# Optimization experiments

Hardware: AMD Instinct MI355X
Metric: run time of the kernel (lower is better)

## Reference

```python
import jax, jax.numpy as jnp
import numpy as np

NEG_SLOPE = 0.2


def gat_conv(h_in, src, dst, W, attn_l, attn_r, num_nodes):
    """DGL-style GATConv: fc -> per-head attention logits -> edge softmax over dst -> scatter-add."""
    H, D = attn_l.shape
    h = (h_in @ W).reshape(num_nodes, H, D)                      # [N,H,D]
    el = jnp.sum(h * attn_l, axis=-1)                            # [N,H]
    er = jnp.sum(h * attn_r, axis=-1)                            # [N,H]
    e = jax.nn.leaky_relu(el[src] + er[dst], NEG_SLOPE)          # [E,H]
    m = jax.ops.segment_max(e, dst, num_segments=num_nodes)      # [N,H]
    m = jnp.where(jnp.isfinite(m), m, 0.0)                       # guard empty segments
    ex = jnp.exp(e - m[dst])                                     # [E,H]
    denom = jax.ops.segment_sum(ex, dst, num_segments=num_nodes) # [N,H]
    a = ex / denom[dst]                                          # [E,H]
    msg = h[src] * a[:, :, None]                                 # [E,H,D]
    out = jax.ops.segment_sum(msg, dst, num_segments=num_nodes)  # [N,H,D]
    return out.reshape(num_nodes, H * D)                         # concat heads


def setup_inputs() -> dict:
    key = jax.random.key(0)
    ks = jax.random.split(key, 12)
    N, E, G = 65536, 1048576, 512
    F_in, H, D = 128, 8, 32
    F_mid = H * D  # 256, concat agg mode
    P = 512
    inp = {
        "node_feats": jax.random.normal(ks[0], (N, F_in), jnp.float32),
        "src": jax.random.randint(ks[1], (E,), 0, N, jnp.int32),
        "dst": jax.random.randint(ks[2], (E,), 0, N, jnp.int32),
        "graph_ids": jnp.sort(jax.random.randint(ks[3], (N,), 0, G, jnp.int32)),
        "num_graphs": G,
        "W0": jax.random.normal(ks[4], (F_in, H * D), jnp.float32) * (1.0 / np.sqrt(F_in)),
        "al0": jax.random.normal(ks[5], (H, D), jnp.float32) * 0.1,
        "ar0": jax.random.normal(ks[6], (H, D), jnp.float32) * 0.1,
        "W1": jax.random.normal(ks[7], (F_mid, H * D), jnp.float32) * (1.0 / np.sqrt(F_mid)),
        "al1": jax.random.normal(ks[8], (H, D), jnp.float32) * 0.1,
        "ar1": jax.random.normal(ks[9], (H, D), jnp.float32) * 0.1,
        "Wd1": jax.random.normal(ks[10], (F_mid, P), jnp.float32) * (1.0 / np.sqrt(F_mid)),
        "bd1": jnp.zeros((P,), jnp.float32),
        "Wd2": jax.random.normal(ks[11], (P, 1), jnp.float32) * (1.0 / np.sqrt(P)),
        "bd2": jnp.zeros((1,), jnp.float32),
    }
    return inp


def reference(node_feats, src, dst, graph_ids, num_graphs,
              W0, al0, ar0, W1, al1, ar1, Wd1, bd1, Wd2, bd2):
    N = node_feats.shape[0]
    # two GATConv message-passing steps with concat head aggregation
    h = gat_conv(node_feats, src, dst, W0, al0, ar0, N)   # [N, 256]
    h = gat_conv(h, src, dst, W1, al1, ar1, N)            # [N, 256]
    # mean readout per graph (AvgPooling)
    sums = jax.ops.segment_sum(h, graph_ids, num_segments=num_graphs)         # [G, 256]
    counts = jax.ops.segment_sum(jnp.ones((N,), h.dtype), graph_ids,
                                 num_segments=num_graphs)                     # [G]
    pooled = sums / jnp.maximum(counts, 1.0)[:, None]
    # predictor MLP: Dense(512, relu) -> Dense(1, linear)
    hidden = jax.nn.relu(pooled @ Wd1 + bd1)
    out = hidden @ Wd2 + bd2                               # [G, 1]
    return out
```

## Files before the change

kernel.cpp:

```cpp
#include <hip/hip_runtime.h>

#define LEAKY 0.2f

typedef unsigned short ushort_t;
typedef __attribute__((ext_vector_type(8))) short short8;
typedef __attribute__((ext_vector_type(4))) float f32x4;

__device__ __forceinline__ unsigned short f2bf(float f) {
  unsigned u = __float_as_uint(f);
  unsigned r = (u + 0x7fff + ((u >> 16) & 1)) >> 16;
  return (unsigned short)r;
}
__device__ __forceinline__ float bf2f(unsigned short u) {
  return __uint_as_float(((unsigned)u) << 16);
}

__global__ void count_k(const int* __restrict__ dst, int* __restrict__ cnt, int E) {
  int i = blockIdx.x * blockDim.x + threadIdx.x;
  if (i < E) atomicAdd(&cnt[dst[i]], 1);
}

__global__ __launch_bounds__(1024) void scan1_k(int* __restrict__ cnt,
                                                int* __restrict__ ptr,
                                                int* __restrict__ bsum, int N) {
  int t = threadIdx.x;
  int i = blockIdx.x * 1024 + t;
  int v = (i < N) ? cnt[i] : 0;
  if (i < N) cnt[i] = 0;
  int lane = t & 63, w = t >> 6;
  int x = v;
  #pragma unroll
  for (int off = 1; off < 64; off <<= 1) {
    int y = __shfl_up(x, off, 64);
    if (lane >= off) x += y;
  }
  __shared__ int wsum[16];
  if (lane == 63) wsum[w] = x;
  __syncthreads();
  if (t < 16) {
    int s = wsum[t];
    #pragma unroll
    for (int off = 1; off < 16; off <<= 1) {
      int y = __shfl_up(s, off, 16);
      if (t >= off) s += y;
    }
    wsum[t] = s;
  }
  __syncthreads();
  int woff = (w > 0) ? wsum[w - 1] : 0;
  int incl = x + woff;
  if (i < N) ptr[i] = incl - v;
  if (t == 1023) bsum[blockIdx.x] = incl;
}

__global__ void scan2_k(int* __restrict__ bsum, int nb) {
  int t = threadIdx.x;
  int v = (t < nb) ? bsum[t] : 0;
  int x = v;
  #pragma unroll
  for (int off = 1; off < 64; off <<= 1) {
    int y = __shfl_up(x, off, 64);
    if (t >= off) x += y;
  }
  if (t < nb) bsum[t] = x - v;
}

__global__ __launch_bounds__(1024) void scan3_k(int* __restrict__ ptr,
                                                const int* __restrict__ bsum,
                                                int N, int E) {
  int i = blockIdx.x * 1024 + threadIdx.x;
  if (i < N) ptr[i] += bsum[blockIdx.x];
  if (i == 0) ptr[N] = E;
}

__global__ void fill_k(const int* __restrict__ dst, const int* __restrict__ src,
                       const int* __restrict__ ptr, int* __restrict__ cur,
                       int* __restrict__ adj, int E) {
  int i = blockIdx.x * blockDim.x + threadIdx.x;
  if (i < E) {
    int d = dst[i];
    int p = atomicAdd(&cur[d], 1);
    adj[ptr[d] + p] = src[i];
  }
}

__global__ void whsplit_k(const float* __restrict__ W, ushort_t* __restrict__ Wh, int K) {
  int i = blockIdx.x * 256 + threadIdx.x;
  if (i >= 256 * K) return;
  int k = i % K, c = i / K;
  Wh[i] = f2bf(W[(long)k * 256 + c]);
}

__global__ __launch_bounds__(256) void asplit_k(const float* __restrict__ A,
                                                ushort_t* __restrict__ Ah,
                                                ushort_t* __restrict__ Al, long total) {
  long i = ((long)blockIdx.x * 256 + threadIdx.x) * 4;
  if (i >= total) return;
  float4 v = *(const float4*)(A + i);
  unsigned short h0 = f2bf(v.x), h1 = f2bf(v.y), h2 = f2bf(v.z), h3 = f2bf(v.w);
  ushort4 hi = make_ushort4(h0, h1, h2, h3);
  ushort4 lo = make_ushort4(f2bf(v.x - bf2f(h0)), f2bf(v.y - bf2f(h1)),
                            f2bf(v.z - bf2f(h2)), f2bf(v.w - bf2f(h3)));
  *(ushort4*)(Ah + i) = hi;
  *(ushort4*)(Al + i) = lo;
}

#define LDT 40
__global__ __launch_bounds__(256) void gemm3_k(const ushort_t* __restrict__ Ahg,
                                               const ushort_t* __restrict__ Alg,
                                               const ushort_t* __restrict__ Bh,
                                               const float* __restrict__ alv,
                                               const float* __restrict__ arv,
                                               ushort_t* __restrict__ C,
                                               float* __restrict__ el,
                                               float* __restrict__ er,
                                               int N, int K) {
  __shared__ ushort_t Ahs[128 * LDT];
  __shared__ ushort_t Als[128 * LDT];
  __shared__ ushort_t Bhs[128 * LDT];
  int t = threadIdx.x;
  int w = t >> 6, l = t & 63;
  long row0 = (long)blockIdx.x * 128;
  int by = blockIdx.y;
  int col0 = by * 128;
  int fr = l & 15;
  int ko = (l >> 4) * 8;
  int ar = t >> 1;
  int ak = (t & 1) * 16;
  int bc = t >> 2;
  int bk = (t & 3) * 8;
  f32x4 acc[2][8] = {};

  for (int k0 = 0; k0 < K; k0 += 32) {
    const ushort_t* ap = Ahg + (row0 + ar) * K + k0 + ak;
    const ushort_t* lp = Alg + (row0 + ar) * K + k0 + ak;
    uint4 ah0 = *(const uint4*)ap;
    uint4 ah1 = *(const uint4*)(ap + 8);
    uint4 al0 = *(const uint4*)lp;
    uint4 al1 = *(const uint4*)(lp + 8);
    uint4 bh0 = *(const uint4*)(Bh + (long)(col0 + bc) * K + k0 + bk);
    uint4 bh1 = *(const uint4*)(Bh + (long)(col0 + bc + 64) * K + k0 + bk);
    __syncthreads();
    *(uint4*)&Ahs[ar * LDT + ak] = ah0;
    *(uint4*)&Ahs[ar * LDT + ak + 8] = ah1;
    *(uint4*)&Als[ar * LDT + ak] = al0;
    *(uint4*)&Als[ar * LDT + ak + 8] = al1;
    *(uint4*)&Bhs[bc * LDT + bk] = bh0;
    *(uint4*)&Bhs[(bc + 64) * LDT + bk] = bh1;
    __syncthreads();
    short8 fah[2], fal[2];
    #pragma unroll
    for (int m = 0; m < 2; ++m) {
      fah[m] = *(const short8*)&Ahs[(w * 32 + m * 16 + fr) * LDT + ko];
      fal[m] = *(const short8*)&Als[(w * 32 + m * 16 + fr) * LDT + ko];
    }
    #pragma unroll
    for (int n = 0; n < 8; ++n) {
      short8 fbh = *(const short8*)&Bhs[(n * 16 + fr) * LDT + ko];
      #pragma unroll
      for (int m = 0; m < 2; ++m) {
        acc[m][n] = __builtin_amdgcn_mfma_f32_16x16x32_bf16(fah[m], fbh, acc[m][n], 0, 0, 0);
        acc[m][n] = __builtin_amdgcn_mfma_f32_16x16x32_bf16(fal[m], fbh, acc[m][n], 0, 0, 0);
      }
    }
  }
  int crow = (l >> 4) * 4;
  float ala[4], alb[4], ara[4], arb[4];
  #pragma unroll
  for (int hd = 0; hd < 4; ++hd) {
    ala[hd] = alv[(4 * by + hd) * 32 + fr];
    alb[hd] = alv[(4 * by + hd) * 32 + 16 + fr];
    ara[hd] = arv[(4 * by + hd) * 32 + fr];
    arb[hd] = arv[(4 * by + hd) * 32 + 16 + fr];
  }
  #pragma unroll
  for (int m = 0; m < 2; ++m) {
    #pragma unroll
    for (int r = 0; r < 4; ++r) {
      long row = row0 + w * 32 + m * 16 + crow + r;
      #pragma unroll
      for (int n = 0; n < 8; ++n)
        C[row * 256 + col0 + n * 16 + fr] = f2bf(acc[m][n][r]);
      #pragma unroll
      for (int hd = 0; hd < 4; ++hd) {
        float pel = acc[m][2 * hd][r] * ala[hd] + acc[m][2 * hd + 1][r] * alb[hd];
        float per = acc[m][2 * hd][r] * ara[hd] + acc[m][2 * hd + 1][r] * arb[hd];
        #pragma unroll
        for (int s = 1; s < 16; s <<= 1) {
          pel += __shfl_xor(pel, s);
          per += __shfl_xor(per, s);
        }
        if (fr == 0) {
          el[row * 8 + 4 * by + hd] = pel;
          er[row * 8 + 4 * by + hd] = per;
        }
      }
    }
  }
}

template <int SPLIT>
__global__ __launch_bounds__(256) void agg_t_k(const ushort_t* __restrict__ hb,
                                               const float* __restrict__ el,
                                               const float* __restrict__ er,
                                               const int* __restrict__ ptr,
                                               const int* __restrict__ adj,
                                               float* __restrict__ outf,
                                               ushort_t* __restrict__ oh,
                                               ushort_t* __restrict__ ol, int N) {
  int wid = threadIdx.x >> 6;
  int l = threadIdx.x & 63;
  int n = blockIdx.x * 4 + wid;
  if (n >= N) return;
  int beg = ptr[n];
  int deg = ptr[n + 1] - beg;
  long obase = (long)n * 256 + l * 4;
  float4 acc = make_float4(0.f, 0.f, 0.f, 0.f);
  if (deg > 0) {
    int hh = l & 7;
    int eo = l >> 3;
    int hg = l >> 3;
    float erv = er[(long)n * 8 + hh];
    if (deg <= 64) {
      int sid = (l < deg) ? adj[beg + l] : 0;
      int npass = (deg + 7) >> 3;
      float v[8];
      float m = -1e30f;
      #pragma unroll
      for (int p = 0; p < 8; ++p) {
        if (p < npass) {
          int e = p * 8 + eo;
          int s = __shfl(sid, e);
          float vv = -1e30f;
          if (e < deg) {
            vv = el[(long)s * 8 + hh] + erv;
            vv = vv > 0.f ? vv : LEAKY * vv;
          }
          v[p] = vv;
          m = fmaxf(m, vv);
        }
      }
      m = fmaxf(m, __shfl_xor(m, 8));
      m = fmaxf(m, __shfl_xor(m, 16));
      m = fmaxf(m, __shfl_xor(m, 32));
      float ssum = 0.f;
      #pragma unroll
      for (int p = 0; p < 8; ++p) {
        if (p < npass) {
          float ex = (p * 8 + eo < deg) ? __expf(v[p] - m) : 0.f;
          v[p] = ex;
          ssum += ex;
        }
      }
      ssum += __shfl_xor(ssum, 8);
      ssum += __shfl_xor(ssum, 16);
      ssum += __shfl_xor(ssum, 32);
      float inv = 1.0f / ssum;
      #pragma unroll
      for (int p = 0; p < 8; ++p) {
        if (p < npass) {
          v[p] *= inv;
          #pragma unroll
          for (int e2 = 0; e2 < 8; ++e2) {
            int e = p * 8 + e2;
            if (e < deg) {
              float a = __shfl(v[p], (e2 << 3) | hg);
              int s = __shfl(sid, e);
              const ushort4 hv = *(const ushort4*)(hb + (long)s * 256 + l * 4);
              acc.x += a * bf2f(hv.x);
              acc.y += a * bf2f(hv.y);
              acc.z += a * bf2f(hv.z);
              acc.w += a * bf2f(hv.w);
            }
          }
        }
      }
    } else {
      float m = -1e30f;
      for (int base = 0; base < deg; base += 8) {
        int e = base + eo;
        float vv = -1e30f;
        if (e < deg) {
          int s = adj[beg + e];
          vv = el[(long)s * 8 + hh] + erv;
          vv = vv > 0.f ? vv : LEAKY * vv;
        }
        m = fmaxf(m, vv);
      }
      m = fmaxf(m, __shfl_xor(m, 8));
      m = fmaxf(m, __shfl_xor(m, 16));
      m = fmaxf(m, __shfl_xor(m, 32));
      float ssum = 0.f;
      for (int base = 0; base < deg; base += 8) {
        int e = base + eo;
        if (e < deg) {
          int s = adj[beg + e];
          float vv = el[(long)s * 8 + hh] + erv;
          vv = vv > 0.f ? vv : LEAKY * vv;
          ssum += __expf(vv - m);
        }
      }
      ssum += __shfl_xor(ssum, 8);
      ssum += __shfl_xor(ssum, 16);
      ssum += __shfl_xor(ssum, 32);
      float inv = 1.0f / ssum;
      for (int base = 0; base < deg; base += 8) {
        int e = base + eo;
        float a_me = 0.f;
        int s_me = 0;
        if (e < deg) {
          s_me = adj[beg + e];
          float vv = el[(long)s_me * 8 + hh] + erv;
          vv = vv > 0.f ? vv : LEAKY * vv;
          a_me = __expf(vv - m) * inv;
        }
        #pragma unroll
        for (int e2 = 0; e2 < 8; ++e2) {
          int e3 = base + e2;
          if (e3 < deg) {
            int srcl = (e2 << 3) | hg;
            float a = __shfl(a_me, srcl);
            int s = __shfl(s_me, srcl);
            const ushort4 hv = *(const ushort4*)(hb + (long)s * 256 + l * 4);
            acc.x += a * bf2f(hv.x);
            acc.y += a * bf2f(hv.y);
            acc.z += a * bf2f(hv.z);
            acc.w += a * bf2f(hv.w);
          }
        }
      }
    }
  }
  if (SPLIT) {
    unsigned short hx = f2bf(acc.x), hy = f2bf(acc.y), hz = f2bf(acc.z), hw = f2bf(acc.w);
    ushort4 hi = make_ushort4(hx, hy, hz, hw);
    ushort4 lo = make_ushort4(f2bf(acc.x - bf2f(hx)), f2bf(acc.y - bf2f(hy)),
                              f2bf(acc.z - bf2f(hz)), f2bf(acc.w - bf2f(hw)));
    *(ushort4*)(oh + obase) = hi;
    *(ushort4*)(ol + obase) = lo;
  } else {
    *(float4*)(outf + obase) = acc;
  }
}

__device__ __forceinline__ int lower_bound_i(const int* a, int n, int key) {
  int lo = 0, hi = n;
  while (lo < hi) {
    int mid = (lo + hi) >> 1;
    if (a[mid] < key) lo = mid + 1; else hi = mid;
  }
  return lo;
}

__global__ __launch_bounds__(256) void poolmlp_k(const float* __restrict__ h,
                                                 const int* __restrict__ gid,
                                                 const float* __restrict__ Wd1,
                                                 const float* __restrict__ bd1,
                                                 const float* __restrict__ Wd2,
                                                 const float* __restrict__ bd2,
                                                 float* __restrict__ outv, int N, int G) {
  int g = blockIdx.x;
  int t = threadIdx.x;
  __shared__ int s_lo, s_hi;
  if (t == 0) {
    s_lo = lower_bound_i(gid, N, g);
    s_hi = lower_bound_i(gid, N, g + 1);
  }
  __syncthreads();
  int lo = s_lo, hi = s_hi;
  float acc = 0.f;
  for (int n = lo; n < hi; ++n) acc += h[(long)n * 256 + t];
  float c = (float)(hi - lo);
  __shared__ float p_s[256];
  __shared__ float red[256];
  p_s[t] = acc / fmaxf(c, 1.f);
  __syncthreads();
  float acc0 = bd1[t], acc1 = bd1[t + 256];
  for (int k = 0; k < 256; ++k) {
    float pv = p_s[k];
    acc0 += pv * Wd1[k * 512 + t];
    acc1 += pv * Wd1[k * 512 + t + 256];
  }
  acc0 = fmaxf(acc0, 0.f);
  acc1 = fmaxf(acc1, 0.f);
  red[t] = acc0 * Wd2[t] + acc1 * Wd2[t + 256];
  __syncthreads();
  for (int off = 128; off > 0; off >>= 1) {
    if (t < off) red[t] += red[t + off];
    __syncthreads();
  }
  if (t == 0) outv[g] = red[0] + bd2[0];
}

extern "C" void kernel_launch(void* const* d_in, const int* in_sizes, int n_in,
                              void* d_out, int out_size, void* d_ws, size_t ws_size,
                              hipStream_t stream) {
  const float* X   = (const float*)d_in[0];
  const int*   src = (const int*)d_in[1];
  const int*   dst = (const int*)d_in[2];
  const int*   gid = (const int*)d_in[3];
  const float* W0  = (const float*)d_in[5];
  const float* al0 = (const float*)d_in[6];
  const float* ar0 = (const float*)d_in[7];
  const float* W1  = (const float*)d_in[8];
  const float* al1 = (const float*)d_in[9];
  const float* ar1 = (const float*)d_in[10];
  const float* Wd1 = (const float*)d_in[11];
  const float* bd1 = (const float*)d_in[12];
  const float* Wd2 = (const float*)d_in[13];
  const float* bd2 = (const float*)d_in[14];

  int E = in_sizes[1];
  int N = in_sizes[3];
  int G = out_size;

  char* w = (char*)d_ws;
  ushort_t* Xh   = (ushort_t*)w;
  ushort_t* Xl   = Xh + (size_t)N * 128;
  ushort_t* Ah   = (ushort_t*)w;
  ushort_t* Al   = Ah + (size_t)N * 256;
  float*    bAgg = (float*)w;
  char* p = w + (size_t)N * 256 * 4;
  ushort_t* hb   = (ushort_t*)p; p += (size_t)N * 256 * 2;
  float*    el   = (float*)p;    p += (size_t)N * 8 * 4;
  float*    er   = (float*)p;    p += (size_t)N * 8 * 4;
  ushort_t* W0h  = (ushort_t*)p; p += (size_t)256 * 128 * 2;
  ushort_t* W1h  = (ushort_t*)p; p += (size_t)256 * 256 * 2;
  int*      ptr  = (int*)p;      p += (size_t)(N + 1) * 4;
  int*      cnt  = (int*)p;      p += (size_t)N * 4;
  int*      adj  = (int*)p;      p += (size_t)E * 4;
  int*      bsum = (int*)p;

  int nb = (N + 1023) / 1024;

  hipMemsetAsync(cnt, 0, (size_t)N * 4, stream);
  count_k<<<(E + 255) / 256, 256, 0, stream>>>(dst, cnt, E);
  scan1_k<<<nb, 1024, 0, stream>>>(cnt, ptr, bsum, N);
  scan2_k<<<1, 64, 0, stream>>>(bsum, nb);
  scan3_k<<<nb, 1024, 0, stream>>>(ptr, bsum, N, E);
  fill_k<<<(E + 255) / 256, 256, 0, stream>>>(dst, src, ptr, cnt, adj, E);

  whsplit_k<<<(256 * 128 + 255) / 256, 256, 0, stream>>>(W0, W0h, 128);
  whsplit_k<<<(256 * 256 + 255) / 256, 256, 0, stream>>>(W1, W1h, 256);
  asplit_k<<<(int)(((long)N * 128 / 4 + 255) / 256), 256, 0, stream>>>(X, Xh, Xl, (long)N * 128);

  dim3 gg(N / 128, 2);
  gemm3_k<<<gg, 256, 0, stream>>>(Xh, Xl, W0h, al0, ar0, hb, el, er, N, 128);
  agg_t_k<1><<<(N + 3) / 4, 256, 0, stream>>>(hb, el, er, ptr, adj, (float*)nullptr, Ah, Al, N);
  gemm3_k<<<gg, 256, 0, stream>>>(Ah, Al, W1h, al1, ar1, hb, el, er, N, 256);
  agg_t_k<0><<<(N + 3) / 4, 256, 0, stream>>>(hb, el, er, ptr, adj, bAgg, (ushort_t*)nullptr, (ushort_t*)nullptr, N);
  poolmlp_k<<<G, 256, 0, stream>>>(bAgg, gid, Wd1, bd1, Wd2, bd2, (float*)d_out, N, G);
}
```

Before: 468.3 us.

## Drop split-bf16 activation precision and widen GEMM tile to full 256 columns

Removes the hi/lo bf16 split of activations, so each GEMM does one MFMA per tile instead of two and reads and writes half the activation bytes in the cast and aggregation kernels. The GEMM now covers all 256 output columns per block (a 2x2 wave layout over a 128x256 tile) instead of two column blocks, so the A tile is loaded from global memory only once. The bf16 output is staged through shared memory so it can be written with coalesced 16-byte stores. The tradeoff is lower accuracy, since activations lose the residual precision the lo part carried, plus more accumulator registers per thread.

```diff
diff --git a/kernel.cpp b/kernel.cpp
--- a/kernel.cpp
+++ b/kernel.cpp
@@ -91,23 +91,16 @@
   Wh[i] = f2bf(W[(long)k * 256 + c]);
 }
 
-__global__ __launch_bounds__(256) void asplit_k(const float* __restrict__ A,
-                                                ushort_t* __restrict__ Ah,
-                                                ushort_t* __restrict__ Al, long total) {
+__global__ __launch_bounds__(256) void acast_k(const float* __restrict__ A,
+                                               ushort_t* __restrict__ Ah, long total) {
   long i = ((long)blockIdx.x * 256 + threadIdx.x) * 4;
   if (i >= total) return;
   float4 v = *(const float4*)(A + i);
-  unsigned short h0 = f2bf(v.x), h1 = f2bf(v.y), h2 = f2bf(v.z), h3 = f2bf(v.w);
-  ushort4 hi = make_ushort4(h0, h1, h2, h3);
-  ushort4 lo = make_ushort4(f2bf(v.x - bf2f(h0)), f2bf(v.y - bf2f(h1)),
-                            f2bf(v.z - bf2f(h2)), f2bf(v.w - bf2f(h3)));
-  *(ushort4*)(Ah + i) = hi;
-  *(ushort4*)(Al + i) = lo;
+  *(ushort4*)(Ah + i) = make_ushort4(f2bf(v.x), f2bf(v.y), f2bf(v.z), f2bf(v.w));
 }
 
 #define LDT 40
-__global__ __launch_bounds__(256) void gemm3_k(const ushort_t* __restrict__ Ahg,
-                                               const ushort_t* __restrict__ Alg,
+__global__ __launch_bounds__(256) void gemm4_k(const ushort_t* __restrict__ Ag,
                                                const ushort_t* __restrict__ Bh,
                                                const float* __restrict__ alv,
                                                const float* __restrict__ arv,
@@ -115,72 +108,64 @@
                                                float* __restrict__ el,
                                                float* __restrict__ er,
                                                int N, int K) {
-  __shared__ ushort_t Ahs[128 * LDT];
-  __shared__ ushort_t Als[128 * LDT];
-  __shared__ ushort_t Bhs[128 * LDT];
+  __shared__ ushort_t smem[128 * LDT + 256 * LDT];
+  ushort_t* As = smem;
+  ushort_t* Bs = smem + 128 * LDT;
   int t = threadIdx.x;
   int w = t >> 6, l = t & 63;
+  int wv_r = w >> 1, wv_c = w & 1;
   long row0 = (long)blockIdx.x * 128;
-  int by = blockIdx.y;
-  int col0 = by * 128;
   int fr = l & 15;
   int ko = (l >> 4) * 8;
+  int crow = (l >> 4) * 4;
   int ar = t >> 1;
   int ak = (t & 1) * 16;
-  int bc = t >> 2;
-  int bk = (t & 3) * 8;
-  f32x4 acc[2][8] = {};
+  int bc = t;
+  f32x4 acc[4][8] = {};
 
   for (int k0 = 0; k0 < K; k0 += 32) {
-    const ushort_t* ap = Ahg + (row0 + ar) * K + k0 + ak;
-    const ushort_t* lp = Alg + (row0 + ar) * K + k0 + ak;
-    uint4 ah0 = *(const uint4*)ap;
-    uint4 ah1 = *(const uint4*)(ap + 8);
-    uint4 al0 = *(const uint4*)lp;
-    uint4 al1 = *(const uint4*)(lp + 8);
-    uint4 bh0 = *(const uint4*)(Bh + (long)(col0 + bc) * K + k0 + bk);
-    uint4 bh1 = *(const uint4*)(Bh + (long)(col0 + bc + 64) * K + k0 + bk);
+    const ushort_t* ap = Ag + (row0 + ar) * K + k0 + ak;
+    uint4 a0 = *(const uint4*)ap;
+    uint4 a1 = *(const uint4*)(ap + 8);
+    const ushort_t* bp = Bh + (long)bc * K + k0;
+    uint4 b0 = *(const uint4*)bp;
+    uint4 b1 = *(const uint4*)(bp + 8);
+    uint4 b2 = *(const uint4*)(bp + 16);
+    uint4 b3 = *(const uint4*)(bp + 24);
     __syncthreads();
-    *(uint4*)&Ahs[ar * LDT + ak] = ah0;
-    *(uint4*)&Ahs[ar * LDT + ak + 8] = ah1;
-    *(uint4*)&Als[ar * LDT + ak] = al0;
-    *(uint4*)&Als[ar * LDT + ak + 8] = al1;
-    *(uint4*)&Bhs[bc * LDT + bk] = bh0;
-    *(uint4*)&Bhs[(bc + 64) * LDT + bk] = bh1;
+    *(uint4*)&As[ar * LDT + ak] = a0;
+    *(uint4*)&As[ar * LDT + ak + 8] = a1;
+    *(uint4*)&Bs[bc * LDT + 0] = b0;
+    *(uint4*)&Bs[bc * LDT + 8] = b1;
+    *(uint4*)&Bs[bc * LDT + 16] = b2;
+    *(uint4*)&Bs[bc * LDT + 24] = b3;
     __syncthreads();
-    short8 fah[2], fal[2];
-    #pragma unroll
-    for (int m = 0; m < 2; ++m) {
-      fah[m] = *(const short8*)&Ahs[(w * 32 + m * 16 + fr) * LDT + ko];
-      fal[m] = *(const short8*)&Als[(w * 32 + m * 16 + fr) * LDT + ko];
+    short8 fah[4];
+    #pragma unroll
+    for (int m = 0; m < 4; ++m)
+      fah[m] = *(const short8*)&As[(wv_r * 64 + m * 16 + fr) * LDT + ko];
+    #pragma unroll
+    for (int n = 0; n < 8; ++n) {
+      short8 fb = *(const short8*)&Bs[(wv_c * 128 + n * 16 + fr) * LDT + ko];
+      #pragma unroll
+      for (int m = 0; m < 4; ++m)
+        acc[m][n] = __builtin_amdgcn_mfma_f32_16x16x32_bf16(fah[m], fb, acc[m][n], 0, 0, 0);
     }
-    #pragma unroll
-    for (int n = 0; n < 8; ++n) {
-      short8 fbh = *(const short8*)&Bhs[(n * 16 + fr) * LDT + ko];
-      #pragma unroll
-      for (int m = 0; m < 2; ++m) {
-        acc[m][n] = __builtin_amdgcn_mfma_f32_16x16x32_bf16(fah[m], fbh, acc[m][n], 0, 0, 0);
-        acc[m][n] = __builtin_amdgcn_mfma_f32_16x16x32_bf16(fal[m], fbh, acc[m][n], 0, 0, 0);
-      }
-    }
-  }
-  int crow = (l >> 4) * 4;
+  }
   float ala[4], alb[4], ara[4], arb[4];
   #pragma unroll
   for (int hd = 0; hd < 4; ++hd) {
-    ala[hd] = alv[(4 * by + hd) * 32 + fr];
-    alb[hd] = alv[(4 * by + hd) * 32 + 16 + fr];
-    ara[hd] = arv[(4 * by + hd) * 32 + fr];
-    arb[hd] = arv[(4 * by + hd) * 32 + 16 + fr];
+    int hbase = (wv_c * 4 + hd) * 32;
+    ala[hd] = alv[hbase + fr];
+    alb[hd] = alv[hbase + 16 + fr];
+    ara[hd] = arv[hbase + fr];
+    arb[hd] = arv[hbase + 16 + fr];
   }
   #pragma unroll
-  for (int m = 0; m < 2; ++m) {
+  for (int m = 0; m < 4; ++m) {
     #pragma unroll
     for (int r = 0; r < 4; ++r) {
-      long row = row0 + w * 32 + m * 16 + crow + r;
-      #pragma unroll
-      for (int n = 0; n < 8; ++n)
-        C[row * 256 + col0 + n * 16 + fr] = f2bf(acc[m][n][r]);
+      long row = row0 + wv_r * 64 + m * 16 + crow + r;
       #pragma unroll
       for (int hd = 0; hd < 4; ++hd) {
         float pel = acc[m][2 * hd][r] * ala[hd] + acc[m][2 * hd + 1][r] * alb[hd];
@@ -191,23 +176,40 @@
           per += __shfl_xor(per, s);
         }
         if (fr == 0) {
-          el[row * 8 + 4 * by + hd] = pel;
-          er[row * 8 + 4 * by + hd] = per;
+          el[row * 8 + wv_c * 4 + hd] = pel;
+          er[row * 8 + wv_c * 4 + hd] = per;
         }
       }
     }
   }
-}
-
-template <int SPLIT>
+  ushort_t* bnc = smem;
+  #pragma unroll
+  for (int m = 0; m < 4; ++m) {
+    __syncthreads();
+    #pragma unroll
+    for (int n = 0; n < 8; ++n)
+      #pragma unroll
+      for (int r = 0; r < 4; ++r)
+        bnc[w * 2048 + (crow + r) * 128 + n * 16 + fr] = f2bf(acc[m][n][r]);
+    __syncthreads();
+    #pragma unroll
+    for (int q = 0; q < 4; ++q) {
+      int idx = q * 64 + l;
+      int rw = idx >> 4, c16 = idx & 15;
+      uint4 v = *(const uint4*)&bnc[w * 2048 + rw * 128 + c16 * 8];
+      *(uint4*)(C + (row0 + wv_r * 64 + m * 16 + rw) * 256 + wv_c * 128 + c16 * 8) = v;
+    }
+  }
+}
+
+template <int OUTBF>
 __global__ __launch_bounds__(256) void agg_t_k(const ushort_t* __restrict__ hb,
                                                const float* __restrict__ el,
                                                const float* __restrict__ er,
                                                const int* __restrict__ ptr,
                                                const int* __restrict__ adj,
                                                float* __restrict__ outf,
-                                               ushort_t* __restrict__ oh,
-                                               ushort_t* __restrict__ ol, int N) {
+                                               ushort_t* __restrict__ oh, int N) {
   int wid = threadIdx.x >> 6;
   int l = threadIdx.x & 63;
   int n = blockIdx.x * 4 + wid;
@@ -331,13 +333,9 @@
       }
     }
   }
-  if (SPLIT) {
-    unsigned short hx = f2bf(acc.x), hy = f2bf(acc.y), hz = f2bf(acc.z), hw = f2bf(acc.w);
-    ushort4 hi = make_ushort4(hx, hy, hz, hw);
-    ushort4 lo = make_ushort4(f2bf(acc.x - bf2f(hx)), f2bf(acc.y - bf2f(hy)),
-                              f2bf(acc.z - bf2f(hz)), f2bf(acc.w - bf2f(hw)));
-    *(ushort4*)(oh + obase) = hi;
-    *(ushort4*)(ol + obase) = lo;
+  if (OUTBF) {
+    *(ushort4*)(oh + obase) =
+        make_ushort4(f2bf(acc.x), f2bf(acc.y), f2bf(acc.z), f2bf(acc.w));
   } else {
     *(float4*)(outf + obase) = acc;
   }
@@ -414,14 +412,11 @@
   int N = in_sizes[3];
   int G = out_size;
 
-  char* w = (char*)d_ws;
-  ushort_t* Xh   = (ushort_t*)w;
-  ushort_t* Xl   = Xh + (size_t)N * 128;
-  ushort_t* Ah   = (ushort_t*)w;
-  ushort_t* Al   = Ah + (size_t)N * 256;
-  float*    bAgg = (float*)w;
-  char* p = w + (size_t)N * 256 * 4;
+  char* p = (char*)d_ws;
+  float*    bAgg = (float*)p;    p += (size_t)N * 256 * 4;
   ushort_t* hb   = (ushort_t*)p; p += (size_t)N * 256 * 2;
+  ushort_t* hagg = (ushort_t*)p; p += (size_t)N * 256 * 2;
+  ushort_t* Xh   = (ushort_t*)p; p += (size_t)N * 128 * 2;
   float*    el   = (float*)p;    p += (size_t)N * 8 * 4;
   float*    er   = (float*)p;    p += (size_t)N * 8 * 4;
   ushort_t* W0h  = (ushort_t*)p; p += (size_t)256 * 128 * 2;
@@ -442,12 +437,11 @@
 
   whsplit_k<<<(256 * 128 + 255) / 256, 256, 0, stream>>>(W0, W0h, 128);
   whsplit_k<<<(256 * 256 + 255) / 256, 256, 0, stream>>>(W1, W1h, 256);
-  asplit_k<<<(int)(((long)N * 128 / 4 + 255) / 256), 256, 0, stream>>>(X, Xh, Xl, (long)N * 128);
-
-  dim3 gg(N / 128, 2);
-  gemm3_k<<<gg, 256, 0, stream>>>(Xh, Xl, W0h, al0, ar0, hb, el, er, N, 128);
-  agg_t_k<1><<<(N + 3) / 4, 256, 0, stream>>>(hb, el, er, ptr, adj, (float*)nullptr, Ah, Al, N);
-  gemm3_k<<<gg, 256, 0, stream>>>(Ah, Al, W1h, al1, ar1, hb, el, er, N, 256);
-  agg_t_k<0><<<(N + 3) / 4, 256, 0, stream>>>(hb, el, er, ptr, adj, bAgg, (ushort_t*)nullptr, (ushort_t*)nullptr, N);
+  acast_k<<<(int)(((long)N * 128 / 4 + 255) / 256), 256, 0, stream>>>(X, Xh, (long)N * 128);
+
+  gemm4_k<<<N / 128, 256, 0, stream>>>(Xh, W0h, al0, ar0, hb, el, er, N, 128);
+  agg_t_k<1><<<(N + 3) / 4, 256, 0, stream>>>(hb, el, er, ptr, adj, (float*)nullptr, hagg, N);
+  gemm4_k<<<N / 128, 256, 0, stream>>>(hagg, W1h, al1, ar1, hb, el, er, N, 256);
+  agg_t_k<0><<<(N + 3) / 4, 256, 0, stream>>>(hb, el, er, ptr, adj, bAgg, (ushort_t*)nullptr, N);
   poolmlp_k<<<G, 256, 0, stream>>>(bAgg, gid, Wd1, bd1, Wd2, bd2, (float*)d_out, N, G);
 }
```

Result: slower. 479.2 us (+2.3%).
